# Performance work log

Hardware: AMD Instinct MI355X
Metric: run time of the kernel (lower is better)

Reference implementation:

```python
import jax, jax.numpy as jnp
import numpy as np

B, DIM, N = 64, 128, 4000
H = 4
DH = DIM // H          # 32
CL = 50                # clusters (hardcoded in module)
K = 9                  # knn_num
SCALOR = DH ** -0.5


def setup_inputs() -> dict:
    key = jax.random.key(0)
    ks = jax.random.split(key, 16)
    s = 0.05
    inp = {
        'x': jax.random.normal(ks[0], (B, DIM, N, 1), jnp.float32),
        # conv_group1 / conv_group2: InstanceNorm(no affine) -> BN(affine) -> ReLU -> 1x1 conv
        'wg1': jax.random.normal(ks[1], (CL, DIM), jnp.float32) * s,
        'bg1': jnp.zeros((CL,), jnp.float32),
        'g1_gamma': jnp.ones((DIM,), jnp.float32),
        'g1_beta': jnp.zeros((DIM,), jnp.float32),
        'wg2': jax.random.normal(ks[2], (CL, DIM), jnp.float32) * s,
        'bg2': jnp.zeros((CL,), jnp.float32),
        'g2_gamma': jnp.ones((DIM,), jnp.float32),
        'g2_beta': jnp.zeros((DIM,), jnp.float32),
        # per-head 1x1 convs (stacked over heads)
        'qkv_w': jax.random.normal(ks[3], (H, DH, DIM), jnp.float32) * s,
        'qkv_b': jnp.zeros((H, DH), jnp.float32),
        'qkv1_w': jax.random.normal(ks[4], (H, 3 * DH, DIM), jnp.float32) * s,
        'qkv1_b': jnp.zeros((H, 3 * DH), jnp.float32),
        # GCBlock convs: conv1 (1,3) stride (1,3): 2*DH->DH ; conv2 (1,3): DH->DH
        'gc1_w': jax.random.normal(ks[5], (H, DH, 2 * DH, 3), jnp.float32) * s,
        'gc1_b': jnp.zeros((H, DH), jnp.float32),
        'gc1_gamma': jnp.ones((H, DH), jnp.float32),
        'gc1_beta': jnp.zeros((H, DH), jnp.float32),
        'gc2_w': jax.random.normal(ks[6], (H, DH, DH, 3), jnp.float32) * s,
        'gc2_b': jnp.zeros((H, DH), jnp.float32),
        'gc2_gamma': jnp.ones((H, DH), jnp.float32),
        'gc2_beta': jnp.zeros((H, DH), jnp.float32),
        # output projections
        'pres_w': jax.random.normal(ks[7], (DIM, 2 * DIM), jnp.float32) * s,
        'pres_b': jnp.zeros((DIM,), jnp.float32),
        'proj_w': jax.random.normal(ks[8], (DIM, DIM), jnp.float32) * s,
        'proj_b': jnp.zeros((DIM,), jnp.float32),
    }
    return inp


def _conv_group(x3, w, bconv, gamma, beta):
    # x3: (b, C, n). InstanceNorm2d(eps=1e-3, no affine) over n, BN(train) over (b,n), ReLU, 1x1 conv.
    mu = x3.mean(-1, keepdims=True)
    var = x3.var(-1, keepdims=True)
    xin = (x3 - mu) * jax.lax.rsqrt(var + 1e-3)
    mu2 = xin.mean((0, 2), keepdims=True)
    var2 = xin.var((0, 2), keepdims=True)
    xbn = gamma[None, :, None] * (xin - mu2) * jax.lax.rsqrt(var2 + 1e-5) + beta[None, :, None]
    xr = jax.nn.relu(xbn)
    return jnp.einsum('oc,bcn->bon', w, xr) + bconv[None, :, None]


def _bn_train(h, gamma, beta, axes):
    mu = h.mean(axes, keepdims=True)
    var = h.var(axes, keepdims=True)
    return gamma * (h - mu) * jax.lax.rsqrt(var + 1e-5) + beta


def _forward(x, wg1, bg1, g1_gamma, g1_beta, wg2, bg2, g2_gamma, g2_beta,
             qkv_w, qkv_b, qkv1_w, qkv1_b,
             gc1_w, gc1_b, gc1_gamma, gc1_beta,
             gc2_w, gc2_b, gc2_gamma, gc2_beta,
             pres_w, pres_b, proj_w, proj_b):
    xs = x[..., 0]                                          # (b, dim, n)
    # cluster assignment 1: softmax over points
    embed1 = _conv_group(xs, wg1, bg1, g1_gamma, g1_beta)   # (b, 50, n)
    S1 = jax.nn.softmax(embed1, axis=2)
    cluster_x = jnp.einsum('bdn,bcn->bdc', xs, S1)          # (b, dim, 50)

    # ---- local branch (per head, vectorized): 1x1 conv -> knn graph feature -> conv stack ----
    q = jnp.einsum('hod,bdc->bhoc', qkv_w, cluster_x) + qkv_b[None, :, :, None]  # (b,H,dh,50)
    xt = q.transpose(0, 1, 3, 2)                            # (b,H,50,dh)
    inner = jnp.einsum('bhnc,bhmc->bhnm', xt, xt)
    sq = jnp.sum(xt * xt, axis=-1)
    pd = 2.0 * inner - sq[..., :, None] - sq[..., None, :]  # negative squared distance
    idx = jax.lax.top_k(pd, K)[1]                            # (b,H,50,K)
    x_exp = jnp.broadcast_to(xt[:, :, None, :, :], xt.shape[:2] + (CL, CL, DH))
    feature = jnp.take_along_axis(x_exp, idx[..., None], axis=3)        # (b,H,50,K,dh)
    center = jnp.broadcast_to(xt[:, :, :, None, :], feature.shape)
    edge = jnp.concatenate([center, center - feature], axis=-1)          # (b,H,50,K,2dh)
    # conv1: kernel (1,3) stride (1,3): K=9 -> 3 windows of 3
    e = edge.reshape(edge.shape[0], H, CL, 3, 3, 2 * DH)
    h1 = jnp.einsum('bhnjti,hoit->bhnjo', e, gc1_w) + gc1_b[None, :, None, None, :]
    h1 = jax.nn.relu(_bn_train(h1, gc1_gamma[None, :, None, None, :], gc1_beta[None, :, None, None, :], (0, 2, 3)))
    # conv2: kernel (1,3): 3 -> 1
    h2 = jnp.einsum('bhnti,hoit->bhno', h1, gc2_w) + gc2_b[None, :, None, :]
    h2 = jax.nn.relu(_bn_train(h2, gc2_gamma[None, :, None, :], gc2_beta[None, :, None, :], (0, 2)))
    local = h2.transpose(0, 1, 3, 2)                        # (b,H,dh,50)

    # ---- global branch: tiny attention over 50 clusters per head ----
    qkv = jnp.einsum('hod,bdc->bhoc', qkv1_w, cluster_x) + qkv1_b[None, :, :, None]  # (b,H,3dh,50)
    qg, kg, vg = jnp.split(qkv, 3, axis=2)
    attn = jax.nn.softmax(SCALOR * jnp.einsum('bhdn,bhdm->bhnm', qg, kg), axis=-1)
    glob = jnp.einsum('bhnm,bhdm->bhdn', attn, vg)          # (b,H,dh,50)

    # interleave [local_h, global_h] per head along channels -> (b, 2*dim, 50)
    per_head = jnp.concatenate([local, glob], axis=2)       # (b,H,2dh,50)
    cat = per_head.reshape(per_head.shape[0], 2 * DIM, CL)
    res = jnp.einsum('oc,bcn->bon', pres_w, cat) + pres_b[None, :, None]  # (b,dim,50)

    # cluster assignment 2: softmax over clusters, scatter back to points
    embed2 = _conv_group(xs, wg2, bg2, g2_gamma, g2_beta)   # (b,50,n)
    S2 = jax.nn.softmax(embed2, axis=1)
    res2 = jnp.einsum('bdc,bcn->bdn', res, S2)              # (b,dim,n)
    out = jnp.einsum('od,bdn->bon', proj_w, res2) + proj_b[None, :, None]
    return out[..., None]                                   # (b,dim,n,1)


def reference(x, wg1, bg1, g1_gamma, g1_beta, wg2, bg2, g2_gamma, g2_beta,
              qkv_w, qkv_b, qkv1_w, qkv1_b,
              gc1_w, gc1_b, gc1_gamma, gc1_beta,
              gc2_w, gc2_b, gc2_gamma, gc2_beta,
              pres_w, pres_b, proj_w, proj_b):
    return _forward(x, wg1, bg1, g1_gamma, g1_beta, wg2, bg2, g2_gamma, g2_beta,
                    qkv_w, qkv_b, qkv1_w, qkv1_b,
                    gc1_w, gc1_b, gc1_gamma, gc1_beta,
                    gc2_w, gc2_b, gc2_gamma, gc2_beta,
                    pres_w, pres_b, proj_w, proj_b)
```

## Files before the change

kernel.cpp:

```cpp
#include <hip/hip_runtime.h>
#include <cstddef>


constexpr size_t O_MU    = 0;
constexpr size_t O_RINV  = 8192;
constexpr size_t O_RATIO = 16384;
constexpr size_t O_A1    = 24576;
constexpr size_t O_B1    = 24704;
constexpr size_t O_A2    = 24832;
constexpr size_t O_B2    = 24960;
constexpr size_t O_PROJWT= 25088;
constexpr size_t O_VPROJ = 41472;
constexpr size_t O_MT    = 41600;
constexpr size_t O_E2    = 74368;
constexpr size_t O_UCXP  = 12874368;
constexpr size_t O_XT    = 17068672;
constexpr size_t O_QT    = 17478272;
constexpr size_t O_KT    = 17887872;
constexpr size_t O_VT    = 18297472;
constexpr size_t O_H1    = 18707072;
constexpr size_t O_P1    = 19935872;
constexpr size_t O_H2    = 19952512;
constexpr size_t O_P2    = 20362112;
constexpr size_t O_CAT   = 20378752;
constexpr size_t O_PRES2 = 21197952;

__global__ __launch_bounds__(256) void k_stats(const float* __restrict__ x,
                                               const float* __restrict__ projw,
                                               float* __restrict__ ws){
  if(blockIdx.x >= 2048){
    int i = (blockIdx.x - 2048)*256 + threadIdx.x;
    int o = i & 127, k = i >> 7;
    ws[O_PROJWT + i] = projw[o*128 + k];
    return;
  }
  int w = threadIdx.x >> 6, lane = threadIdx.x & 63;
  int row = blockIdx.x*4 + w;
  const float4* xr = (const float4*)(x + (size_t)row * 4000);
  float s = 0.f, sq = 0.f;
  for(int i = lane; i < 1000; i += 64){
    float4 v = xr[i];
    s  += v.x + v.y + v.z + v.w;
    sq += v.x*v.x + v.y*v.y + v.z*v.z + v.w*v.w;
  }
  for(int off = 32; off > 0; off >>= 1){
    s  += __shfl_down(s,  off, 64);
    sq += __shfl_down(sq, off, 64);
  }
  if(lane == 0){
    float mean = s * (1.f/4000.f);
    float var  = sq * (1.f/4000.f) - mean*mean;
    ws[O_MU   + row] = mean;
    ws[O_RINV + row] = rsqrtf(var + 1e-3f);
    ws[O_RATIO+ row] = var / (var + 1e-3f);
  }
}

__global__ __launch_bounds__(256) void k_mprep(const float* __restrict__ presw,
                                               const float* __restrict__ presb,
                                               const float* __restrict__ g1g,
                                               const float* __restrict__ g1b,
                                               const float* __restrict__ g2g,
                                               const float* __restrict__ g2b,
                                               float* __restrict__ ws){
  int t = threadIdx.x;
  if(blockIdx.x < 128){
    int kk2 = blockIdx.x * 2;
    __shared__ float pwc[2][128];
    { int which = t >> 7, d = t & 127; pwc[which][d] = presw[d*256 + kk2 + which]; }
    __syncthreads();
    int which = t >> 7, o = t & 127;
    float acc = 0.f;
    for(int d = 0; d < 128; d++) acc += ws[O_PROJWT + d*128 + o] * pwc[which][d];
    ws[O_MT + (size_t)(kk2 + which)*128 + o] = acc;
  }else if(blockIdx.x == 128){
    if(t < 128){
      float v = 0.f;
      for(int d = 0; d < 128; d++) v += ws[O_PROJWT + d*128 + t] * presb[d];
      ws[O_VPROJ + t] = v;
    }
  }else{
    if(t < 128){
      float s = 0.f;
      for(int b = 0; b < 64; b++) s += ws[O_RATIO + b*128 + t];
      float var2 = s * (1.f/64.f);
      float inv2 = rsqrtf(var2 + 1e-5f);
      ws[O_A1+t] = g1g[t] * inv2;  ws[O_B1+t] = g1b[t];
      ws[O_A2+t] = g2g[t] * inv2;  ws[O_B2+t] = g2b[t];
    }
  }
}

__global__ __launch_bounds__(512, 4) void k_e1ucx(const float* __restrict__ x,
    const float* __restrict__ wg1, const float* __restrict__ bg1,
    float* __restrict__ ws){
  int ch = blockIdx.x, b = blockIdx.y;
  __shared__ float lW1[128*52];
  __shared__ float lrv1[128*48];
  __shared__ float lxt [48*128];
  __shared__ float ca1[128], cb1[128];
  __shared__ float bg1p[56];
  int t = threadIdx.x;
  if(t < 128){
    float mu = ws[O_MU + b*128 + t], ri = ws[O_RINV + b*128 + t];
    float a1 = ws[O_A1+t]*ri;
    ca1[t] = a1; cb1[t] = ws[O_B1+t] - a1*mu;
  }
  if(t >= 448 && t < 504){ int q = t - 448; bg1p[q] = (q < 50) ? bg1[q] : 0.f; }
  for(int i = t; i < 1664; i += 512){
    int cl = i >> 5, cq = i & 31;
    float4 w = (cl < 50) ? *(const float4*)&wg1[cl*128 + cq*4] : make_float4(0.f,0.f,0.f,0.f);
    int c0 = cq*4;
    lW1[(c0+0)*52+cl] = w.x; lW1[(c0+1)*52+cl] = w.y;
    lW1[(c0+2)*52+cl] = w.z; lW1[(c0+3)*52+cl] = w.w;
  }
  int dg = t & 31, cg = t >> 5;
  int d4 = dg*4, c4 = cg*4;
  float ua[4][4];
  #pragma unroll
  for(int r = 0; r < 4; r++){ ua[r][0]=0.f; ua[r][1]=0.f; ua[r][2]=0.f; ua[r][3]=0.f; }
  float zacc = 0.f;
  int ig = t >> 4, jg = t & 15;
  int clb = ig*2, j4 = jg*4;
  int sc[3], sj[3], cx[3];
  float4 pf[3];
  #pragma unroll
  for(int j = 0; j < 3; j++){
    int i = t + 512*j;
    sc[j] = i/12; sj[j] = (i%12)*4;
    cx[j] = sc[j] ^ (((sj[j] >> 2) & 7) << 2);
  }
  #pragma unroll
  for(int j = 0; j < 3; j++)
    pf[j] = *(const float4*)&x[(size_t)(b*128 + sc[j])*4000 + ch*500 + sj[j]];

  for(int st = 0; st < 11; st++){
    int lim = (st == 10) ? 20 : 48;
    __syncthreads();
    #pragma unroll
    for(int j = 0; j < 3; j++){
      int c = sc[j], jj = sj[j], cxx = cx[j];
      float4 xv = (jj < lim) ? pf[j] : make_float4(0.f,0.f,0.f,0.f);
      lxt[(jj+0)*128 + cxx] = xv.x; lxt[(jj+1)*128 + cxx] = xv.y;
      lxt[(jj+2)*128 + cxx] = xv.z; lxt[(jj+3)*128 + cxx] = xv.w;
      float a1 = ca1[c], b1v = cb1[c];
      float4 r1;
      r1.x = fmaxf(a1*xv.x + b1v, 0.f); r1.y = fmaxf(a1*xv.y + b1v, 0.f);
      r1.z = fmaxf(a1*xv.z + b1v, 0.f); r1.w = fmaxf(a1*xv.w + b1v, 0.f);
      *(float4*)&lrv1[c*48 + jj] = r1;
    }
    __syncthreads();
    if(st < 10){
      int lim2 = (st == 9) ? 20 : 48;
      int nb2 = ch*500 + (st+1)*48;
      #pragma unroll
      for(int j = 0; j < 3; j++)
        pf[j] = (sj[j] < lim2) ? *(const float4*)&x[(size_t)(b*128 + sc[j])*4000 + nb2 + sj[j]]
                               : make_float4(0.f,0.f,0.f,0.f);
    }
    float e[2][4];
    if(ig < 26 && jg < 12){
      e[0][0]=0.f; e[0][1]=0.f; e[0][2]=0.f; e[0][3]=0.f;
      e[1][0]=0.f; e[1][1]=0.f; e[1][2]=0.f; e[1][3]=0.f;
      #pragma unroll 4
      for(int c = 0; c < 128; c++){
        float2 w = *(const float2*)&lW1[c*52 + clb];
        float4 v = *(const float4*)&lrv1[c*48 + j4];
        e[0][0] += w.x*v.x; e[0][1] += w.x*v.y; e[0][2] += w.x*v.z; e[0][3] += w.x*v.w;
        e[1][0] += w.y*v.x; e[1][1] += w.y*v.y; e[1][2] += w.y*v.z; e[1][3] += w.y*v.w;
      }
    }
    __syncthreads();
    if(ig < 26 && jg < 12){
      bool live = (j4 < lim);
      #pragma unroll
      for(int r = 0; r < 2; r++){
        float bias = bg1p[clb + r];
        float4 u = make_float4(0.f,0.f,0.f,0.f);
        if(live){
          u.x = expf(e[r][0] + bias); u.y = expf(e[r][1] + bias);
          u.z = expf(e[r][2] + bias); u.w = expf(e[r][3] + bias);
        }
        *(float4*)&lrv1[(clb + r)*48 + j4] = u;
      }
    }
    __syncthreads();
    if(cg < 14){
      #pragma unroll 2
      for(int n4 = 0; n4 < 12; n4++){
        int n0 = n4*4;
        int dx = d4 ^ ((n4 & 7) << 2);
        float4 u0 = *(const float4*)&lrv1[(c4+0)*48 + n0];
        float4 u1 = *(const float4*)&lrv1[(c4+1)*48 + n0];
        float4 u2 = *(const float4*)&lrv1[(c4+2)*48 + n0];
        float4 u3 = *(const float4*)&lrv1[(c4+3)*48 + n0];
        float4 x0 = *(const float4*)&lxt[(n0+0)*128 + dx];
        float4 x1 = *(const float4*)&lxt[(n0+1)*128 + dx];
        float4 x2 = *(const float4*)&lxt[(n0+2)*128 + dx];
        float4 x3 = *(const float4*)&lxt[(n0+3)*128 + dx];
        #define ACC4(r, XC) \
          ua[r][0] += x0.XC*u0.x + x1.XC*u0.y + x2.XC*u0.z + x3.XC*u0.w; \
          ua[r][1] += x0.XC*u1.x + x1.XC*u1.y + x2.XC*u1.z + x3.XC*u1.w; \
          ua[r][2] += x0.XC*u2.x + x1.XC*u2.y + x2.XC*u2.z + x3.XC*u2.w; \
          ua[r][3] += x0.XC*u3.x + x1.XC*u3.y + x2.XC*u3.z + x3.XC*u3.w;
        ACC4(0, x) ACC4(1, y) ACC4(2, z) ACC4(3, w)
        #undef ACC4
      }
    }
    if(t < 52){
      float s = 0.f;
      #pragma unroll
      for(int k = 0; k < 12; k++){
        float4 u = *(const float4*)&lrv1[t*48 + k*4];
        s += u.x + u.y + u.z + u.w;
      }
      zacc += s;
    }
  }
  if(cg < 14){
    #pragma unroll
    for(int r = 0; r < 4; r++){
      size_t base = O_UCXP + ((size_t)(ch*64 + b)*132 + d4 + r)*56 + c4;
      *(float4*)&ws[base] = make_float4(ua[r][0], ua[r][1], ua[r][2], ua[r][3]);
    }
  }
  if(t < 52) ws[O_UCXP + ((size_t)(ch*64 + b)*132 + 128)*56 + t] = zacc;
}

__global__ __launch_bounds__(512, 6) void k_e2(const float* __restrict__ x,
    const float* __restrict__ wg2, const float* __restrict__ bg2,
    float* __restrict__ ws){
  int ch = blockIdx.x, b = blockIdx.y;
  __shared__ float lW2[128*52];
  __shared__ float lrv2[128*48];
  __shared__ float ca2[128], cb2[128];
  __shared__ float bg2p[56];
  int t = threadIdx.x;
  if(t < 128){
    float mu = ws[O_MU + b*128 + t], ri = ws[O_RINV + b*128 + t];
    float a2 = ws[O_A2+t]*ri;
    ca2[t] = a2; cb2[t] = ws[O_B2+t] - a2*mu;
  }
  if(t >= 448 && t < 504){ int q = t - 448; bg2p[q] = (q < 50) ? bg2[q] : 0.f; }
  for(int i = t; i < 1664; i += 512){
    int cl = i >> 5, cq = i & 31;
    float4 w = (cl < 50) ? *(const float4*)&wg2[cl*128 + cq*4] : make_float4(0.f,0.f,0.f,0.f);
    int c0 = cq*4;
    lW2[(c0+0)*52+cl] = w.x; lW2[(c0+1)*52+cl] = w.y;
    lW2[(c0+2)*52+cl] = w.z; lW2[(c0+3)*52+cl] = w.w;
  }
  int ig = t >> 4, jg = t & 15;
  int clb = ig*2, j4 = jg*4;
  int sc[3], sj[3];
  float4 pf[3];
  #pragma unroll
  for(int j = 0; j < 3; j++){ int i = t + 512*j; sc[j] = i/12; sj[j] = (i%12)*4; }
  {
    int nb0 = ch*336;
    int lim0 = 4000 - nb0; if(lim0 > 48) lim0 = 48;
    #pragma unroll
    for(int j = 0; j < 3; j++)
      pf[j] = (sj[j] < lim0) ? *(const float4*)&x[(size_t)(b*128 + sc[j])*4000 + nb0 + sj[j]]
                             : make_float4(0.f,0.f,0.f,0.f);
  }
  for(int st = 0; st < 7; st++){
    int nb = ch*336 + st*48;
    int lim = 4000 - nb; if(lim > 48) lim = 48;
    __syncthreads();
    #pragma unroll
    for(int j = 0; j < 3; j++){
      int c = sc[j], jj = sj[j];
      float4 xv = (jj < lim) ? pf[j] : make_float4(0.f,0.f,0.f,0.f);
      float a2 = ca2[c], b2v = cb2[c];
      float4 r2;
      r2.x = fmaxf(a2*xv.x + b2v, 0.f); r2.y = fmaxf(a2*xv.y + b2v, 0.f);
      r2.z = fmaxf(a2*xv.z + b2v, 0.f); r2.w = fmaxf(a2*xv.w + b2v, 0.f);
      *(float4*)&lrv2[c*48 + jj] = r2;
    }
    __syncthreads();
    if(st < 6){
      int nb2 = nb + 48;
      int lim2 = 4000 - nb2; if(lim2 > 48) lim2 = 48;
      #pragma unroll
      for(int j = 0; j < 3; j++)
        pf[j] = (sj[j] < lim2) ? *(const float4*)&x[(size_t)(b*128 + sc[j])*4000 + nb2 + sj[j]]
                               : make_float4(0.f,0.f,0.f,0.f);
    }
    if(ig < 26 && jg < 12){
      float e[2][4];
      e[0][0]=0.f; e[0][1]=0.f; e[0][2]=0.f; e[0][3]=0.f;
      e[1][0]=0.f; e[1][1]=0.f; e[1][2]=0.f; e[1][3]=0.f;
      #pragma unroll 4
      for(int c = 0; c < 128; c++){
        float2 w = *(const float2*)&lW2[c*52 + clb];
        float4 v = *(const float4*)&lrv2[c*48 + j4];
        e[0][0] += w.x*v.x; e[0][1] += w.x*v.y; e[0][2] += w.x*v.z; e[0][3] += w.x*v.w;
        e[1][0] += w.y*v.x; e[1][1] += w.y*v.y; e[1][2] += w.y*v.z; e[1][3] += w.y*v.w;
      }
      if(j4 < lim){
        #pragma unroll
        for(int r = 0; r < 2; r++){
          int cl = clb + r;
          if(cl < 50){
            float bias = bg2p[cl];
            float4 o = make_float4(e[r][0]+bias, e[r][1]+bias, e[r][2]+bias, e[r][3]+bias);
            *(float4*)&ws[O_E2 + ((size_t)b*50 + cl)*4000 + nb + j4] = o;
          }
        }
      }
    }
  }
}

__global__ __launch_bounds__(256) void k_qkv(const float* __restrict__ qw,
                                             const float* __restrict__ qb,
                                             const float* __restrict__ q1w,
                                             const float* __restrict__ q1b,
                                             float* __restrict__ ws){
  int rt = blockIdx.x, b = blockIdx.y;
  __shared__ float wl[64*130];
  __shared__ float cxl[128*52];
  __shared__ float zi[52];
  int t = threadIdx.x;
  if(t < 52){
    float s = 0.f;
    if(t < 50){
      #pragma unroll
      for(int ch = 0; ch < 8; ch++)
        s += ws[O_UCXP + ((size_t)(ch*64 + b)*132 + 128)*56 + t];
      zi[t] = 1.f / s;
    }else zi[t] = 0.f;
  }
  for(int i = t; i < 2048; i += 256){
    int rl = i >> 5, kq = i & 31, row = rt*64 + rl;
    float4 w = (row < 128) ? *(const float4*)&qw[row*128 + kq*4]
                           : *(const float4*)&q1w[(row-128)*128 + kq*4];
    int k0 = kq*4;
    wl[rl*130 + k0+0] = w.x; wl[rl*130 + k0+1] = w.y;
    wl[rl*130 + k0+2] = w.z; wl[rl*130 + k0+3] = w.w;
  }
  __syncthreads();
  for(int i = t; i < 6656; i += 256){
    int k = i / 52, c = i % 52;
    float s = 0.f;
    size_t base = O_UCXP + ((size_t)b*132 + k)*56 + c;
    #pragma unroll
    for(int ch = 0; ch < 8; ch++) s += ws[base + (size_t)ch*64*132*56];
    cxl[i] = s * zi[c];
  }
  __syncthreads();
  int ig = t & 15, cg = t >> 4;
  float acc[4][4];
  #pragma unroll
  for(int r = 0; r < 4; r++){ acc[r][0]=0.f; acc[r][1]=0.f; acc[r][2]=0.f; acc[r][3]=0.f; }
  if(cg < 13){
    int rb = ig*4, cb = cg*4;
    #pragma unroll 4
    for(int k = 0; k < 128; k++){
      float4 cv = *(const float4*)&cxl[k*52 + cb];
      float w0 = wl[(rb+0)*130 + k], w1 = wl[(rb+1)*130 + k];
      float w2 = wl[(rb+2)*130 + k], w3 = wl[(rb+3)*130 + k];
      acc[0][0] += w0*cv.x; acc[0][1] += w0*cv.y; acc[0][2] += w0*cv.z; acc[0][3] += w0*cv.w;
      acc[1][0] += w1*cv.x; acc[1][1] += w1*cv.y; acc[1][2] += w1*cv.z; acc[1][3] += w1*cv.w;
      acc[2][0] += w2*cv.x; acc[2][1] += w2*cv.y; acc[2][2] += w2*cv.z; acc[2][3] += w2*cv.w;
      acc[3][0] += w3*cv.x; acc[3][1] += w3*cv.y; acc[3][2] += w3*cv.z; acc[3][3] += w3*cv.w;
    }
    #pragma unroll
    for(int r = 0; r < 4; r++){
      int row = rt*64 + ig*4 + r;
      size_t base; float bias;
      if(row < 128){
        int h = row >> 5;
        bias = qb[row];
        base = O_XT + (size_t)(b*4 + h)*1600 + (row & 31);
      }else{
        int r2 = row - 128, h = r2/96, j = r2%96, kind = j >> 5, dd = j & 31;
        bias = q1b[r2];
        base = (kind==0 ? O_QT : kind==1 ? O_KT : O_VT) + (size_t)(b*4 + h)*1600 + dd;
      }
      #pragma unroll
      for(int s = 0; s < 4; s++){
        int c = cg*4 + s;
        if(c < 50) ws[base + (size_t)c*32] = acc[r][s] + bias;
      }
    }
  }
}

__global__ __launch_bounds__(256) void k_knn(const float* __restrict__ g1w,
                                             const float* __restrict__ g1bias,
                                             float* __restrict__ ws){
  int h = blockIdx.x, b = blockIdx.y;
  __shared__ float xtl[50][33];
  __shared__ float pdl[50][52];
  __shared__ float sql[50];
  __shared__ int   idxl[50][9];
  __shared__ float w1l[6144];
  int t = threadIdx.x;
  const float* xtg = ws + O_XT + (size_t)(b*4 + h)*1600;
  for(int i = t; i < 1600; i += 256) xtl[i >> 5][i & 31] = xtg[i];
  for(int i = t; i < 6144; i += 256){
    int o = i / 192, r = i % 192, ii = r / 3, tt = r % 3;
    w1l[(ii*3 + tt)*32 + o] = g1w[(size_t)h*6144 + i];
  }
  __syncthreads();
  if(t < 50){
    float s = 0.f;
    for(int d = 0; d < 32; d++){ float v = xtl[t][d]; s += v*v; }
    sql[t] = s;
  }
  __syncthreads();
  for(int i = t; i < 2500; i += 256){
    int n = i / 50, m = i % 50;
    float s = 0.f;
    for(int d = 0; d < 32; d++) s += xtl[n][d]*xtl[m][d];
    pdl[n][m] = 2.f*s - sql[n] - sql[m];
  }
  __syncthreads();
  if(t < 50){
    float pv = INFINITY; int pi = -1;
    for(int k = 0; k < 9; k++){
      float bv = -INFINITY; int bi = 1000;
      for(int m = 0; m < 50; m++){
        float v = pdl[t][m];
        bool elig = (v < pv) || (v == pv && m > pi);
        if(elig && (v > bv || (v == bv && m < bi))){ bv = v; bi = m; }
      }
      idxl[t][k] = bi; pv = bv; pi = bi;
    }
  }
  __syncthreads();
  float acc[32];
  bool act = (t < 150);
  if(act){
    int n = t / 3, jw = t % 3;
    #pragma unroll
    for(int o = 0; o < 32; o++) acc[o] = 0.f;
    for(int t3 = 0; t3 < 3; t3++){
      int kx = idxl[n][jw*3 + t3];
      for(int ii = 0; ii < 32; ii++){
        float c0 = xtl[n][ii];
        float c1 = c0 - xtl[kx][ii];
        const float* wr0 = w1l + (ii*3 + t3)*32;
        const float* wr1 = w1l + ((ii+32)*3 + t3)*32;
        #pragma unroll
        for(int o = 0; o < 32; o++) acc[o] += c0*wr0[o] + c1*wr1[o];
      }
    }
    float* out = ws + O_H1 + ((size_t)(b*4 + h)*150 + n*3 + jw)*32;
    #pragma unroll
    for(int o = 0; o < 32; o++){ acc[o] += g1bias[h*32 + o]; out[o] = acc[o]; }
  }
  __syncthreads();
  if(act){
    #pragma unroll
    for(int o = 0; o < 32; o++) w1l[t*32 + o] = acc[o];
  }
  __syncthreads();
  {
    int o = t & 31, part = t >> 5;
    float s = 0.f, sq = 0.f;
    for(int r = part; r < 150; r += 8){
      float v = w1l[r*32 + o];
      s += v; sq += v*v;
    }
    float* sp = &pdl[0][0];
    sp[part*32 + o] = s; sp[256 + part*32 + o] = sq;
    __syncthreads();
    if(t < 32){
      float S = 0.f, Q = 0.f;
      for(int p = 0; p < 8; p++){ S += sp[p*32 + t]; Q += sp[256 + p*32 + t]; }
      ws[O_P1 + b*256 + h*32 + t]       = S;
      ws[O_P1 + b*256 + 128 + h*32 + t] = Q;
    }
  }
}

__global__ __launch_bounds__(256) void k_conv2(const float* __restrict__ g1g,
                                               const float* __restrict__ g1be,
                                               const float* __restrict__ g2w,
                                               const float* __restrict__ g2bias,
                                               float* __restrict__ ws){
  int h = blockIdx.x, b = blockIdx.y;
  __shared__ float hl[150][33];
  __shared__ float w2l[3072];
  __shared__ float rs[8][32], rq[8][32];
  __shared__ float b1s[32], b1t[32];
  int t = threadIdx.x;
  if(t < 32){
    float s = 0.f, sq = 0.f;
    for(int bb = 0; bb < 64; bb++){
      s  += ws[O_P1 + bb*256 + h*32 + t];
      sq += ws[O_P1 + bb*256 + 128 + h*32 + t];
    }
    float mean = s * (1.f/9600.f), var = sq * (1.f/9600.f) - mean*mean;
    float sc = g1g[h*32+t] * rsqrtf(var + 1e-5f);
    b1s[t] = sc; b1t[t] = g1be[h*32+t] - sc*mean;
  }
  for(int i = t; i < 3072; i += 256){
    int o = i / 96, r = i % 96, ii = r / 3, tt = r % 3;
    w2l[(ii*3 + tt)*32 + o] = g2w[(size_t)h*3072 + i];
  }
  __syncthreads();
  const float* h1p = ws + O_H1 + (size_t)(b*4 + h)*4800;
  for(int i = t; i < 4800; i += 256){
    int nj = i >> 5, ii = i & 31;
    hl[nj][ii] = fmaxf(b1s[ii]*h1p[i] + b1t[ii], 0.f);
  }
  __syncthreads();
  int o = t & 31, ng = t >> 5;
  float bias = g2bias[h*32 + o];
  float s = 0.f, sq = 0.f;
  for(int n = ng; n < 50; n += 8){
    float acc = 0.f;
    for(int t3 = 0; t3 < 3; t3++){
      const float* hr = hl[n*3 + t3];
      #pragma unroll
      for(int ii = 0; ii < 32; ii++) acc += hr[ii] * w2l[(ii*3 + t3)*32 + o];
    }
    acc += bias;
    ws[O_H2 + ((size_t)(b*4 + h)*50 + n)*32 + o] = acc;
    s += acc; sq += acc*acc;
  }
  rs[ng][o] = s; rq[ng][o] = sq; __syncthreads();
  if(t < 32){
    float S = 0.f, Q = 0.f;
    for(int g2 = 0; g2 < 8; g2++){ S += rs[g2][t]; Q += rq[g2][t]; }
    ws[O_P2 + (b*4 + h)*64 + t]      = S;
    ws[O_P2 + (b*4 + h)*64 + 32 + t] = Q;
  }
}

__global__ __launch_bounds__(256) void k_attn(const float* __restrict__ g2g,
                                              const float* __restrict__ g2be,
                                              float* __restrict__ ws){
  int h = blockIdx.x, b = blockIdx.y;
  __shared__ float qtl[50][33], ktl[50][33], vtl[50][33], al[50][52];
  __shared__ float b2s[32], b2t[32];
  int t = threadIdx.x;
  if(t < 32){
    float s = 0.f, sq = 0.f;
    for(int bb = 0; bb < 64; bb++){
      s  += ws[O_P2 + (size_t)(bb*4 + h)*64 + t];
      sq += ws[O_P2 + (size_t)(bb*4 + h)*64 + 32 + t];
    }
    float mean = s * (1.f/3200.f), var = sq * (1.f/3200.f) - mean*mean;
    float sc = g2g[h*32+t] * rsqrtf(var + 1e-5f);
    b2s[t] = sc; b2t[t] = g2be[h*32+t] - sc*mean;
  }
  size_t base = (size_t)(b*4 + h)*1600;
  for(int i = t; i < 1600; i += 256){
    int n = i >> 5, d = i & 31;
    qtl[n][d] = ws[O_QT + base + i];
    ktl[n][d] = ws[O_KT + base + i];
    vtl[n][d] = ws[O_VT + base + i];
  }
  __syncthreads();
  for(int i = t; i < 2500; i += 256){
    int n = i / 50, m = i % 50;
    float s = 0.f;
    for(int d = 0; d < 32; d++) s += qtl[n][d]*ktl[m][d];
    al[n][m] = s * 0.17677669529663687f;
  }
  __syncthreads();
  if(t < 50){
    float m = -INFINITY;
    for(int j = 0; j < 50; j++) m = fmaxf(m, al[t][j]);
    float s = 0.f;
    for(int j = 0; j < 50; j++){ float e = expf(al[t][j] - m); al[t][j] = e; s += e; }
    float inv = 1.f/s;
    for(int j = 0; j < 50; j++) al[t][j] *= inv;
  }
  __syncthreads();
  for(int i = t; i < 1600; i += 256){
    int n = i >> 5, d = i & 31;
    float gacc = 0.f;
    for(int m = 0; m < 50; m++) gacc += al[n][m]*vtl[m][d];
    ws[O_CAT + ((size_t)b*256 + h*64 + 32 + d)*50 + n] = gacc;
    float l = fmaxf(b2s[d]*ws[O_H2 + ((size_t)(b*4 + h)*50 + n)*32 + d] + b2t[d], 0.f);
    ws[O_CAT + ((size_t)b*256 + h*64 + d)*50 + n] = l;
  }
}

__global__ __launch_bounds__(256) void k_res(float* __restrict__ ws){
  int oh = blockIdx.x & 1, b = blockIdx.x >> 1;
  __shared__ float mtl[64*68];
  __shared__ float catl[64*52];
  __shared__ float vp[64];
  int t = threadIdx.x;
  if(t < 64) vp[t] = ws[O_VPROJ + oh*64 + t];
  int og = t >> 4, cg = t & 15;
  int ob = og*4, cb = cg*4;
  float acc[4][4];
  #pragma unroll
  for(int r = 0; r < 4; r++){ acc[r][0]=0.f; acc[r][1]=0.f; acc[r][2]=0.f; acc[r][3]=0.f; }
  for(int kc = 0; kc < 4; kc++){
    int k0 = kc*64;
    __syncthreads();
    for(int i = t; i < 1024; i += 256){
      int k = i >> 4, oq = i & 15;
      float4 m = *(const float4*)&ws[O_MT + (size_t)(k0 + k)*128 + oh*64 + oq*4];
      *(float4*)&mtl[k*68 + oq*4] = m;
    }
    for(int i = t; i < 3328; i += 256){
      int k = i / 52, c = i % 52;
      catl[i] = (c < 50) ? ws[O_CAT + (size_t)b*12800 + (k0 + k)*50 + c] : 0.f;
    }
    __syncthreads();
    if(cg < 13){
      #pragma unroll 2
      for(int k = 0; k < 64; k++){
        float4 m0 = *(const float4*)&mtl[k*68 + ob];
        float4 cv = *(const float4*)&catl[k*52 + cb];
        acc[0][0] += m0.x*cv.x; acc[0][1] += m0.x*cv.y; acc[0][2] += m0.x*cv.z; acc[0][3] += m0.x*cv.w;
        acc[1][0] += m0.y*cv.x; acc[1][1] += m0.y*cv.y; acc[1][2] += m0.y*cv.z; acc[1][3] += m0.y*cv.w;
        acc[2][0] += m0.z*cv.x; acc[2][1] += m0.z*cv.y; acc[2][2] += m0.z*cv.z; acc[2][3] += m0.z*cv.w;
        acc[3][0] += m0.w*cv.x; acc[3][1] += m0.w*cv.y; acc[3][2] += m0.w*cv.z; acc[3][3] += m0.w*cv.w;
      }
    }
  }
  if(cg < 13){
    #pragma unroll
    for(int s = 0; s < 4; s++){
      int c = cb + s;
      if(c < 50){
        float4 o0 = make_float4(acc[0][s]+vp[ob+0], acc[1][s]+vp[ob+1], acc[2][s]+vp[ob+2], acc[3][s]+vp[ob+3]);
        *(float4*)&ws[O_PRES2 + (size_t)b*6400 + c*128 + oh*64 + ob] = o0;
      }
    }
  }
}

__global__ __launch_bounds__(256) void k_out(const float* __restrict__ projb,
                                             float* __restrict__ ws,
                                             float* __restrict__ out){
  int nt = blockIdx.x, b = blockIdx.y;
  int n0 = nt*64;
  __shared__ float sl[50*64];
  __shared__ float p2l[50*132];
  __shared__ float pb[128];
  int t = threadIdx.x;
  for(int i = t; i < 3200; i += 256){
    int c = i >> 6, j = i & 63, n = n0 + j;
    sl[i] = (n < 4000) ? ws[O_E2 + ((size_t)b*50 + c)*4000 + n] : 0.f;
  }
  for(int i = t; i < 6400; i += 256){
    int c = i >> 7, o = i & 127;
    p2l[c*132 + o] = ws[O_PRES2 + (size_t)b*6400 + c*128 + o];
  }
  if(t < 128) pb[t] = projb[t];
  __syncthreads();
  if(t < 64){
    int j = t;
    float m = -INFINITY;
    for(int c = 0; c < 50; c++) m = fmaxf(m, sl[c*64 + j]);
    float s = 0.f;
    for(int c = 0; c < 50; c++){ float e = expf(sl[c*64 + j] - m); sl[c*64 + j] = e; s += e; }
    float inv = 1.f/s;
    for(int c = 0; c < 50; c++) sl[c*64 + j] *= inv;
  }
  __syncthreads();
  int og = t >> 4, jg = t & 15;
  int ob = og*8, j4 = jg*4;
  float acc[8][4];
  #pragma unroll
  for(int r = 0; r < 8; r++){ acc[r][0]=0.f; acc[r][1]=0.f; acc[r][2]=0.f; acc[r][3]=0.f; }
  #pragma unroll 2
  for(int c = 0; c < 50; c++){
    float4 sv = *(const float4*)&sl[c*64 + j4];
    float4 p0 = *(const float4*)&p2l[c*132 + ob];
    float4 p1 = *(const float4*)&p2l[c*132 + ob + 4];
    acc[0][0] += p0.x*sv.x; acc[0][1] += p0.x*sv.y; acc[0][2] += p0.x*sv.z; acc[0][3] += p0.x*sv.w;
    acc[1][0] += p0.y*sv.x; acc[1][1] += p0.y*sv.y; acc[1][2] += p0.y*sv.z; acc[1][3] += p0.y*sv.w;
    acc[2][0] += p0.z*sv.x; acc[2][1] += p0.z*sv.y; acc[2][2] += p0.z*sv.z; acc[2][3] += p0.z*sv.w;
    acc[3][0] += p0.w*sv.x; acc[3][1] += p0.w*sv.y; acc[3][2] += p0.w*sv.z; acc[3][3] += p0.w*sv.w;
    acc[4][0] += p1.x*sv.x; acc[4][1] += p1.x*sv.y; acc[4][2] += p1.x*sv.z; acc[4][3] += p1.x*sv.w;
    acc[5][0] += p1.y*sv.x; acc[5][1] += p1.y*sv.y; acc[5][2] += p1.y*sv.z; acc[5][3] += p1.y*sv.w;
    acc[6][0] += p1.z*sv.x; acc[6][1] += p1.z*sv.y; acc[6][2] += p1.z*sv.z; acc[6][3] += p1.z*sv.w;
    acc[7][0] += p1.w*sv.x; acc[7][1] += p1.w*sv.y; acc[7][2] += p1.w*sv.z; acc[7][3] += p1.w*sv.w;
  }
  int n = n0 + j4;
  if(n < 4000){
    #pragma unroll
    for(int r = 0; r < 8; r++){
      float bv = pb[ob + r];
      float4 o = make_float4(acc[r][0]+bv, acc[r][1]+bv, acc[r][2]+bv, acc[r][3]+bv);
      *(float4*)&out[(size_t)(b*128 + ob + r)*4000 + n] = o;
    }
  }
}

extern "C" void kernel_launch(void* const* d_in, const int* in_sizes, int n_in,
                              void* d_out, int out_size, void* d_ws, size_t ws_size,
                              hipStream_t stream){
  (void)in_sizes; (void)n_in; (void)out_size; (void)ws_size;
  const float* x      = (const float*)d_in[0];
  const float* wg1    = (const float*)d_in[1];
  const float* bg1    = (const float*)d_in[2];
  const float* g1g    = (const float*)d_in[3];
  const float* g1b    = (const float*)d_in[4];
  const float* wg2    = (const float*)d_in[5];
  const float* bg2    = (const float*)d_in[6];
  const float* g2g    = (const float*)d_in[7];
  const float* g2b    = (const float*)d_in[8];
  const float* qkvw   = (const float*)d_in[9];
  const float* qkvb   = (const float*)d_in[10];
  const float* qkv1w  = (const float*)d_in[11];
  const float* qkv1b  = (const float*)d_in[12];
  const float* gc1w   = (const float*)d_in[13];
  const float* gc1bias= (const float*)d_in[14];
  const float* gc1g   = (const float*)d_in[15];
  const float* gc1be  = (const float*)d_in[16];
  const float* gc2w   = (const float*)d_in[17];
  const float* gc2bias= (const float*)d_in[18];
  const float* gc2g   = (const float*)d_in[19];
  const float* gc2be  = (const float*)d_in[20];
  const float* presw  = (const float*)d_in[21];
  const float* presb  = (const float*)d_in[22];
  const float* projw  = (const float*)d_in[23];
  const float* projb  = (const float*)d_in[24];
  float* ws = (float*)d_ws;
  float* out = (float*)d_out;

  k_stats<<<2112, 256, 0, stream>>>(x, projw, ws);
  k_mprep<<<130, 256, 0, stream>>>(presw, presb, g1g, g1b, g2g, g2b, ws);
  k_e1ucx<<<dim3(8, 64), 512, 0, stream>>>(x, wg1, bg1, ws);
  k_e2<<<dim3(12, 64), 512, 0, stream>>>(x, wg2, bg2, ws);
  k_qkv<<<dim3(8, 64), 256, 0, stream>>>(qkvw, qkvb, qkv1w, qkv1b, ws);
  k_knn<<<dim3(4, 64), 256, 0, stream>>>(gc1w, gc1bias, ws);
  k_conv2<<<dim3(4, 64), 256, 0, stream>>>(gc1g, gc1be, gc2w, gc2bias, ws);
  k_attn<<<dim3(4, 64), 256, 0, stream>>>(gc2g, gc2be, ws);
  k_res<<<128, 256, 0, stream>>>(ws);
  k_out<<<dim3(63, 64), 256, 0, stream>>>(projb, ws, out);
}
```

Before: 787.6 us.

## Pretranspose cluster weights globally and retile e1/e2 kernels with 256-thread blocks

```diff
diff --git a/kernel.cpp b/kernel.cpp
--- a/kernel.cpp
+++ b/kernel.cpp
@@ -14,20 +14,33 @@
 constexpr size_t O_MT    = 41600;
 constexpr size_t O_E2    = 74368;
 constexpr size_t O_UCXP  = 12874368;
-constexpr size_t O_XT    = 17068672;
-constexpr size_t O_QT    = 17478272;
-constexpr size_t O_KT    = 17887872;
-constexpr size_t O_VT    = 18297472;
-constexpr size_t O_H1    = 18707072;
-constexpr size_t O_P1    = 19935872;
-constexpr size_t O_H2    = 19952512;
-constexpr size_t O_P2    = 20362112;
-constexpr size_t O_CAT   = 20378752;
-constexpr size_t O_PRES2 = 21197952;
+constexpr size_t O_W1T   = 18551424;
+constexpr size_t O_W2T   = 18558080;
+constexpr size_t O_XT    = 18564736;
+constexpr size_t O_QT    = 18974336;
+constexpr size_t O_KT    = 19383936;
+constexpr size_t O_VT    = 19793536;
+constexpr size_t O_H1    = 20203136;
+constexpr size_t O_P1    = 21431936;
+constexpr size_t O_H2    = 21448320;
+constexpr size_t O_P2    = 21857920;
+constexpr size_t O_CAT   = 21874240;
+constexpr size_t O_PRES2 = 22693440;
 
 __global__ __launch_bounds__(256) void k_stats(const float* __restrict__ x,
                                                const float* __restrict__ projw,
+                                               const float* __restrict__ wg1,
+                                               const float* __restrict__ wg2,
                                                float* __restrict__ ws){
+  if(blockIdx.x >= 2112){
+    const float* src = (blockIdx.x == 2112) ? wg1 : wg2;
+    size_t dst = (blockIdx.x == 2112) ? O_W1T : O_W2T;
+    for(int i = threadIdx.x; i < 6656; i += 256){
+      int c = i / 52, cl = i % 52;
+      ws[dst + i] = (cl < 50) ? src[cl*128 + c] : 0.f;
+    }
+    return;
+  }
   if(blockIdx.x >= 2048){
     int i = (blockIdx.x - 2048)*256 + threadIdx.x;
     int o = i & 127, k = i >> 7;
@@ -91,11 +104,9 @@
   }
 }
 
-__global__ __launch_bounds__(512, 4) void k_e1ucx(const float* __restrict__ x,
-    const float* __restrict__ wg1, const float* __restrict__ bg1,
-    float* __restrict__ ws){
+__global__ __launch_bounds__(256, 3) void k_e1ucx(const float* __restrict__ x,
+    const float* __restrict__ bg1, float* __restrict__ ws){
   int ch = blockIdx.x, b = blockIdx.y;
-  __shared__ float lW1[128*52];
   __shared__ float lrv1[128*48];
   __shared__ float lxt [48*128];
   __shared__ float ca1[128], cb1[128];
@@ -106,39 +117,40 @@
     float a1 = ws[O_A1+t]*ri;
     ca1[t] = a1; cb1[t] = ws[O_B1+t] - a1*mu;
   }
-  if(t >= 448 && t < 504){ int q = t - 448; bg1p[q] = (q < 50) ? bg1[q] : 0.f; }
-  for(int i = t; i < 1664; i += 512){
-    int cl = i >> 5, cq = i & 31;
-    float4 w = (cl < 50) ? *(const float4*)&wg1[cl*128 + cq*4] : make_float4(0.f,0.f,0.f,0.f);
-    int c0 = cq*4;
-    lW1[(c0+0)*52+cl] = w.x; lW1[(c0+1)*52+cl] = w.y;
-    lW1[(c0+2)*52+cl] = w.z; lW1[(c0+3)*52+cl] = w.w;
-  }
+  if(t >= 192 && t < 248){ int q = t - 192; bg1p[q] = (q < 50) ? bg1[q] : 0.f; }
+  const float* W1T = ws + O_W1T;
   int dg = t & 31, cg = t >> 5;
-  int d4 = dg*4, c4 = cg*4;
-  float ua[4][4];
+  int d4 = dg*4, c8 = cg*8;
+  float ua[4][8];
   #pragma unroll
-  for(int r = 0; r < 4; r++){ ua[r][0]=0.f; ua[r][1]=0.f; ua[r][2]=0.f; ua[r][3]=0.f; }
+  for(int r = 0; r < 4; r++)
+    #pragma unroll
+    for(int i = 0; i < 8; i++) ua[r][i] = 0.f;
   float zacc = 0.f;
   int ig = t >> 4, jg = t & 15;
-  int clb = ig*2, j4 = jg*4;
-  int sc[3], sj[3], cx[3];
-  float4 pf[3];
+  int clb = ig*4, j4 = jg*4;
+  int sc[6], sj[6], cx[6];
+  float4 pf[6];
   #pragma unroll
-  for(int j = 0; j < 3; j++){
-    int i = t + 512*j;
+  for(int j = 0; j < 6; j++){
+    int i = t + 256*j;
     sc[j] = i/12; sj[j] = (i%12)*4;
     cx[j] = sc[j] ^ (((sj[j] >> 2) & 7) << 2);
   }
-  #pragma unroll
-  for(int j = 0; j < 3; j++)
-    pf[j] = *(const float4*)&x[(size_t)(b*128 + sc[j])*4000 + ch*500 + sj[j]];
-
-  for(int st = 0; st < 11; st++){
-    int lim = (st == 10) ? 20 : 48;
-    __syncthreads();
-    #pragma unroll
-    for(int j = 0; j < 3; j++){
+  {
+    int nb0 = ch*336;
+    int lim0 = 4000 - nb0; if(lim0 > 48) lim0 = 48;
+    #pragma unroll
+    for(int j = 0; j < 6; j++)
+      pf[j] = (sj[j] < lim0) ? *(const float4*)&x[(size_t)(b*128 + sc[j])*4000 + nb0 + sj[j]]
+                             : make_float4(0.f,0.f,0.f,0.f);
+  }
+
+  for(int st = 0; st < 7; st++){
+    int lim = 4000 - (ch*336 + st*48); if(lim > 48) lim = 48;
+    __syncthreads();
+    #pragma unroll
+    for(int j = 0; j < 6; j++){
       int c = sc[j], jj = sj[j], cxx = cx[j];
       float4 xv = (jj < lim) ? pf[j] : make_float4(0.f,0.f,0.f,0.f);
       lxt[(jj+0)*128 + cxx] = xv.x; lxt[(jj+1)*128 + cxx] = xv.y;
@@ -150,31 +162,33 @@
       *(float4*)&lrv1[c*48 + jj] = r1;
     }
     __syncthreads();
-    if(st < 10){
-      int lim2 = (st == 9) ? 20 : 48;
-      int nb2 = ch*500 + (st+1)*48;
-      #pragma unroll
-      for(int j = 0; j < 3; j++)
+    if(st < 6){
+      int nb2 = ch*336 + (st+1)*48;
+      int lim2 = 4000 - nb2; if(lim2 > 48) lim2 = 48;
+      #pragma unroll
+      for(int j = 0; j < 6; j++)
         pf[j] = (sj[j] < lim2) ? *(const float4*)&x[(size_t)(b*128 + sc[j])*4000 + nb2 + sj[j]]
                                : make_float4(0.f,0.f,0.f,0.f);
     }
-    float e[2][4];
-    if(ig < 26 && jg < 12){
-      e[0][0]=0.f; e[0][1]=0.f; e[0][2]=0.f; e[0][3]=0.f;
-      e[1][0]=0.f; e[1][1]=0.f; e[1][2]=0.f; e[1][3]=0.f;
+    float e[4][4];
+    if(ig < 13 && jg < 12){
+      #pragma unroll
+      for(int r = 0; r < 4; r++){ e[r][0]=0.f; e[r][1]=0.f; e[r][2]=0.f; e[r][3]=0.f; }
       #pragma unroll 4
       for(int c = 0; c < 128; c++){
-        float2 w = *(const float2*)&lW1[c*52 + clb];
+        float4 w = *(const float4*)&W1T[c*52 + clb];
         float4 v = *(const float4*)&lrv1[c*48 + j4];
         e[0][0] += w.x*v.x; e[0][1] += w.x*v.y; e[0][2] += w.x*v.z; e[0][3] += w.x*v.w;
         e[1][0] += w.y*v.x; e[1][1] += w.y*v.y; e[1][2] += w.y*v.z; e[1][3] += w.y*v.w;
-      }
-    }
-    __syncthreads();
-    if(ig < 26 && jg < 12){
+        e[2][0] += w.z*v.x; e[2][1] += w.z*v.y; e[2][2] += w.z*v.z; e[2][3] += w.z*v.w;
+        e[3][0] += w.w*v.x; e[3][1] += w.w*v.y; e[3][2] += w.w*v.z; e[3][3] += w.w*v.w;
+      }
+    }
+    __syncthreads();
+    if(ig < 13 && jg < 12){
       bool live = (j4 < lim);
       #pragma unroll
-      for(int r = 0; r < 2; r++){
+      for(int r = 0; r < 4; r++){
         float bias = bg1p[clb + r];
         float4 u = make_float4(0.f,0.f,0.f,0.f);
         if(live){
@@ -185,26 +199,25 @@
       }
     }
     __syncthreads();
-    if(cg < 14){
+    if(cg < 7){
       #pragma unroll 2
       for(int n4 = 0; n4 < 12; n4++){
         int n0 = n4*4;
         int dx = d4 ^ ((n4 & 7) << 2);
-        float4 u0 = *(const float4*)&lrv1[(c4+0)*48 + n0];
-        float4 u1 = *(const float4*)&lrv1[(c4+1)*48 + n0];
-        float4 u2 = *(const float4*)&lrv1[(c4+2)*48 + n0];
-        float4 u3 = *(const float4*)&lrv1[(c4+3)*48 + n0];
+        float4 uv[8];
+        #pragma unroll
+        for(int i = 0; i < 8; i++) uv[i] = *(const float4*)&lrv1[(c8 + i)*48 + n0];
         float4 x0 = *(const float4*)&lxt[(n0+0)*128 + dx];
         float4 x1 = *(const float4*)&lxt[(n0+1)*128 + dx];
         float4 x2 = *(const float4*)&lxt[(n0+2)*128 + dx];
         float4 x3 = *(const float4*)&lxt[(n0+3)*128 + dx];
-        #define ACC4(r, XC) \
-          ua[r][0] += x0.XC*u0.x + x1.XC*u0.y + x2.XC*u0.z + x3.XC*u0.w; \
-          ua[r][1] += x0.XC*u1.x + x1.XC*u1.y + x2.XC*u1.z + x3.XC*u1.w; \
-          ua[r][2] += x0.XC*u2.x + x1.XC*u2.y + x2.XC*u2.z + x3.XC*u2.w; \
-          ua[r][3] += x0.XC*u3.x + x1.XC*u3.y + x2.XC*u3.z + x3.XC*u3.w;
-        ACC4(0, x) ACC4(1, y) ACC4(2, z) ACC4(3, w)
-        #undef ACC4
+        #pragma unroll
+        for(int i = 0; i < 8; i++){
+          ua[0][i] += x0.x*uv[i].x + x1.x*uv[i].y + x2.x*uv[i].z + x3.x*uv[i].w;
+          ua[1][i] += x0.y*uv[i].x + x1.y*uv[i].y + x2.y*uv[i].z + x3.y*uv[i].w;
+          ua[2][i] += x0.z*uv[i].x + x1.z*uv[i].y + x2.z*uv[i].z + x3.z*uv[i].w;
+          ua[3][i] += x0.w*uv[i].x + x1.w*uv[i].y + x2.w*uv[i].z + x3.w*uv[i].w;
+        }
       }
     }
     if(t < 52){
@@ -217,21 +230,20 @@
       zacc += s;
     }
   }
-  if(cg < 14){
+  if(cg < 7){
     #pragma unroll
     for(int r = 0; r < 4; r++){
-      size_t base = O_UCXP + ((size_t)(ch*64 + b)*132 + d4 + r)*56 + c4;
-      *(float4*)&ws[base] = make_float4(ua[r][0], ua[r][1], ua[r][2], ua[r][3]);
+      size_t base = O_UCXP + ((size_t)(ch*64 + b)*132 + d4 + r)*56 + c8;
+      *(float4*)&ws[base]     = make_float4(ua[r][0], ua[r][1], ua[r][2], ua[r][3]);
+      *(float4*)&ws[base + 4] = make_float4(ua[r][4], ua[r][5], ua[r][6], ua[r][7]);
     }
   }
   if(t < 52) ws[O_UCXP + ((size_t)(ch*64 + b)*132 + 128)*56 + t] = zacc;
 }
 
-__global__ __launch_bounds__(512, 6) void k_e2(const float* __restrict__ x,
-    const float* __restrict__ wg2, const float* __restrict__ bg2,
-    float* __restrict__ ws){
+__global__ __launch_bounds__(256, 6) void k_e2(const float* __restrict__ x,
+    const float* __restrict__ bg2, float* __restrict__ ws){
   int ch = blockIdx.x, b = blockIdx.y;
-  __shared__ float lW2[128*52];
   __shared__ float lrv2[128*48];
   __shared__ float ca2[128], cb2[128];
   __shared__ float bg2p[56];
@@ -241,34 +253,28 @@
     float a2 = ws[O_A2+t]*ri;
     ca2[t] = a2; cb2[t] = ws[O_B2+t] - a2*mu;
   }
-  if(t >= 448 && t < 504){ int q = t - 448; bg2p[q] = (q < 50) ? bg2[q] : 0.f; }
-  for(int i = t; i < 1664; i += 512){
-    int cl = i >> 5, cq = i & 31;
-    float4 w = (cl < 50) ? *(const float4*)&wg2[cl*128 + cq*4] : make_float4(0.f,0.f,0.f,0.f);
-    int c0 = cq*4;
-    lW2[(c0+0)*52+cl] = w.x; lW2[(c0+1)*52+cl] = w.y;
-    lW2[(c0+2)*52+cl] = w.z; lW2[(c0+3)*52+cl] = w.w;
-  }
+  if(t >= 192 && t < 248){ int q = t - 192; bg2p[q] = (q < 50) ? bg2[q] : 0.f; }
+  const float* W2T = ws + O_W2T;
   int ig = t >> 4, jg = t & 15;
-  int clb = ig*2, j4 = jg*4;
-  int sc[3], sj[3];
-  float4 pf[3];
+  int clb = ig*4, j4 = jg*4;
+  int sc[6], sj[6];
+  float4 pf[6];
   #pragma unroll
-  for(int j = 0; j < 3; j++){ int i = t + 512*j; sc[j] = i/12; sj[j] = (i%12)*4; }
+  for(int j = 0; j < 6; j++){ int i = t + 256*j; sc[j] = i/12; sj[j] = (i%12)*4; }
   {
-    int nb0 = ch*336;
+    int nb0 = ch*168;
     int lim0 = 4000 - nb0; if(lim0 > 48) lim0 = 48;
     #pragma unroll
-    for(int j = 0; j < 3; j++)
+    for(int j = 0; j < 6; j++)
       pf[j] = (sj[j] < lim0) ? *(const float4*)&x[(size_t)(b*128 + sc[j])*4000 + nb0 + sj[j]]
                              : make_float4(0.f,0.f,0.f,0.f);
   }
-  for(int st = 0; st < 7; st++){
-    int nb = ch*336 + st*48;
+  for(int st = 0; st < 4; st++){
+    int nb = ch*168 + st*48;
     int lim = 4000 - nb; if(lim > 48) lim = 48;
     __syncthreads();
     #pragma unroll
-    for(int j = 0; j < 3; j++){
+    for(int j = 0; j < 6; j++){
       int c = sc[j], jj = sj[j];
       float4 xv = (jj < lim) ? pf[j] : make_float4(0.f,0.f,0.f,0.f);
       float a2 = ca2[c], b2v = cb2[c];
@@ -278,28 +284,30 @@
       *(float4*)&lrv2[c*48 + jj] = r2;
     }
     __syncthreads();
-    if(st < 6){
+    if(st < 3){
       int nb2 = nb + 48;
       int lim2 = 4000 - nb2; if(lim2 > 48) lim2 = 48;
       #pragma unroll
-      for(int j = 0; j < 3; j++)
+      for(int j = 0; j < 6; j++)
         pf[j] = (sj[j] < lim2) ? *(const float4*)&x[(size_t)(b*128 + sc[j])*4000 + nb2 + sj[j]]
                                : make_float4(0.f,0.f,0.f,0.f);
     }
-    if(ig < 26 && jg < 12){
-      float e[2][4];
-      e[0][0]=0.f; e[0][1]=0.f; e[0][2]=0.f; e[0][3]=0.f;
-      e[1][0]=0.f; e[1][1]=0.f; e[1][2]=0.f; e[1][3]=0.f;
+    if(ig < 13 && jg < 12 && lim > 0){
+      float e[4][4];
+      #pragma unroll
+      for(int r = 0; r < 4; r++){ e[r][0]=0.f; e[r][1]=0.f; e[r][2]=0.f; e[r][3]=0.f; }
       #pragma unroll 4
       for(int c = 0; c < 128; c++){
-        float2 w = *(const float2*)&lW2[c*52 + clb];
+        float4 w = *(const float4*)&W2T[c*52 + clb];
         float4 v = *(const float4*)&lrv2[c*48 + j4];
         e[0][0] += w.x*v.x; e[0][1] += w.x*v.y; e[0][2] += w.x*v.z; e[0][3] += w.x*v.w;
         e[1][0] += w.y*v.x; e[1][1] += w.y*v.y; e[1][2] += w.y*v.z; e[1][3] += w.y*v.w;
+        e[2][0] += w.z*v.x; e[2][1] += w.z*v.y; e[2][2] += w.z*v.z; e[2][3] += w.z*v.w;
+        e[3][0] += w.w*v.x; e[3][1] += w.w*v.y; e[3][2] += w.w*v.z; e[3][3] += w.w*v.w;
       }
       if(j4 < lim){
         #pragma unroll
-        for(int r = 0; r < 2; r++){
+        for(int r = 0; r < 4; r++){
           int cl = clb + r;
           if(cl < 50){
             float bias = bg2p[cl];
@@ -326,7 +334,7 @@
     float s = 0.f;
     if(t < 50){
       #pragma unroll
-      for(int ch = 0; ch < 8; ch++)
+      for(int ch = 0; ch < 12; ch++)
         s += ws[O_UCXP + ((size_t)(ch*64 + b)*132 + 128)*56 + t];
       zi[t] = 1.f / s;
     }else zi[t] = 0.f;
@@ -345,7 +353,7 @@
     float s = 0.f;
     size_t base = O_UCXP + ((size_t)b*132 + k)*56 + c;
     #pragma unroll
-    for(int ch = 0; ch < 8; ch++) s += ws[base + (size_t)ch*64*132*56];
+    for(int ch = 0; ch < 12; ch++) s += ws[base + (size_t)ch*473088];
     cxl[i] = s * zi[c];
   }
   __syncthreads();
@@ -722,10 +730,10 @@
   float* ws = (float*)d_ws;
   float* out = (float*)d_out;
 
-  k_stats<<<2112, 256, 0, stream>>>(x, projw, ws);
+  k_stats<<<2114, 256, 0, stream>>>(x, projw, wg1, wg2, ws);
   k_mprep<<<130, 256, 0, stream>>>(presw, presb, g1g, g1b, g2g, g2b, ws);
-  k_e1ucx<<<dim3(8, 64), 512, 0, stream>>>(x, wg1, bg1, ws);
-  k_e2<<<dim3(12, 64), 512, 0, stream>>>(x, wg2, bg2, ws);
+  k_e1ucx<<<dim3(12, 64), 256, 0, stream>>>(x, bg1, ws);
+  k_e2<<<dim3(24, 64), 256, 0, stream>>>(x, bg2, ws);
   k_qkv<<<dim3(8, 64), 256, 0, stream>>>(qkvw, qkvb, qkv1w, qkv1b, ws);
   k_knn<<<dim3(4, 64), 256, 0, stream>>>(gc1w, gc1bias, ws);
   k_conv2<<<dim3(4, 64), 256, 0, stream>>>(gc1g, gc1be, gc2w, gc2bias, ws);
```

New measurement: 924.4 us. 1.17x slower.
